# Kernel optimization log

Measured on AMD Instinct MI355X. Metric: run time of the kernel, lower is better.

## Reference

```python
import jax, jax.numpy as jnp
import numpy as np

N = 100000   # nodes
E = 1600000  # edges
R = 500      # relation types
D = 128      # in_ent_feats == out_ent_feats
H = 8        # heads
Dh = 16      # head dim
DFF = 4 * D  # feed-forward hidden
HOPS = 5
ALPHA = 0.15
SLOPE = 0.2
EPS = 1e-5


def setup_inputs() -> dict:
    key = jax.random.key(0)
    ks = jax.random.split(key, 12)
    s = 0.05  # small-init scale
    return {
        "ent_feat": jax.random.normal(ks[0], (N, D), jnp.float32),
        "rel_feat": jax.random.normal(ks[1], (R, D), jnp.float32),
        "src": jax.random.randint(ks[2], (E,), 0, N),
        "dst": jax.random.randint(ks[3], (E,), 0, N),
        "e_type": jax.random.randint(ks[4], (E,), 0, R),
        "ln1_g": jnp.ones((D,), jnp.float32),
        "ln1_b": jnp.zeros((D,), jnp.float32),
        "W_ent": jax.random.normal(ks[5], (D, H * Dh), jnp.float32) * s,
        "W_rel": jax.random.normal(ks[6], (D, H * Dh), jnp.float32) * s,
        "attn_h": jax.random.normal(ks[7], (1, H, Dh), jnp.float32) * s,
        "attn_t": jax.random.normal(ks[8], (1, H, Dh), jnp.float32) * s,
        "attn_r": jax.random.normal(ks[9], (1, H, Dh), jnp.float32) * s,
        "ln2_g": jnp.ones((H * Dh,), jnp.float32),
        "ln2_b": jnp.zeros((H * Dh,), jnp.float32),
        "W1": jax.random.normal(ks[10], (H * Dh, DFF), jnp.float32) * s,
        "b1": jnp.zeros((DFF,), jnp.float32),
        "W2": jax.random.normal(ks[11], (DFF, H * Dh), jnp.float32) * s,
        "b2": jnp.zeros((H * Dh,), jnp.float32),
    }


def _ln(x, g, b):
    mu = x.mean(-1, keepdims=True)
    var = x.var(-1, keepdims=True)
    return (x - mu) * jax.lax.rsqrt(var + EPS) * g + b


def reference(ent_feat, rel_feat, src, dst, e_type,
              ln1_g, ln1_b, W_ent, W_rel, attn_h, attn_t, attn_r,
              ln2_g, ln2_b, W1, b1, W2, b2):
    # graph layer norm (dropout is identity at eval)
    h = _ln(ent_feat, ln1_g, ln1_b)                       # [N, D]
    feat = (h @ W_ent).reshape(N, H, Dh)                  # [N, H, Dh]
    frel = (rel_feat @ W_rel).reshape(R, H, Dh)           # [R, H, Dh]
    eh = (feat * attn_h).sum(-1)                          # [N, H]
    et = (feat * attn_t).sum(-1)                          # [N, H]
    er = (frel * attn_r).sum(-1)[e_type]                  # [E, H]
    # edge scores: u_add_v + relation term, leaky relu
    e = eh[src] + et[dst] + er                            # [E, H]
    e = jnp.where(e > 0, e, SLOPE * e)
    # edge softmax over incoming edges of each dst node
    m = jax.ops.segment_max(e, dst, num_segments=N)       # [N, H]
    ex = jnp.exp(e - m[dst])
    ssum = jax.ops.segment_sum(ex, dst, num_segments=N)
    a = ex / ssum[dst]                                    # [E, H]
    # PPR diffusion
    feat0 = feat
    f = feat0
    for _ in range(HOPS):
        msg = f[src] * a[:, :, None]                      # [E, H, Dh]
        agg = jax.ops.segment_sum(msg, dst, num_segments=N)
        f = (1.0 - ALPHA) * agg + ALPHA * feat0
    # residual (Identity since in == out)
    rst = f + h.reshape(N, H, Dh)
    rst = rst.reshape(N, H * Dh)
    # feed-forward sublayer with residual
    y = _ln(rst, ln2_g, ln2_b)
    ff = jax.nn.relu(y @ W1 + b1) @ W2 + b2
    return ff + rst
```

## Files before the change

### kernel.cpp

```cpp
#include <hip/hip_runtime.h>
#include <hip/hip_bf16.h>
#include <math.h>

#define N_NODES 100000
#define N_EDGES 1600000
#define N_REL   500
#define DIM     128
#define NHEAD   8
#define DFF     512
#define ALPHA   0.15f
#define SLOPE   0.2f
#define LN_EPS  1e-5f

#define SCHUNK   1024
#define NSCANBLK ((N_NODES + SCHUNK - 1) / SCHUNK)

#define NWIN    8
#define WNODES  12500
#define NECHUNK 256
#define ECHUNK  (N_EDGES / NECHUNK)

#define FNODES  16

typedef unsigned short u16;
typedef unsigned int   u32;

typedef __attribute__((ext_vector_type(8))) short  bf16x8;
typedef __attribute__((ext_vector_type(4))) float  f32x4;

__device__ __forceinline__ float bf2f(u16 u) {
    return __uint_as_float(((u32)u) << 16);
}
__device__ __forceinline__ u16 f2bf(float f) {
    __hip_bfloat16 b = __float2bfloat16(f);
    return *reinterpret_cast<u16*>(&b);
}

__global__ void zero_k(int* __restrict__ p, int n) {
    int i = blockIdx.x * blockDim.x + threadIdx.x;
    if (i < n) p[i] = 0;
}

__global__ void swz1_k(const float* __restrict__ W1, u16* __restrict__ W1s) {
    const int i = blockIdx.x * 256 + threadIdx.x;
    const int k = i >> 9, n = i & 511;
    W1s[n * DIM + k] = f2bf(W1[i]);
}
__global__ void swz2_k(const float* __restrict__ W2, u16* __restrict__ W2s) {
    const int i = blockIdx.x * 256 + threadIdx.x;
    const int k = i >> 7, n = i & 127;
    W2s[n * DFF + k] = f2bf(W2[i]);
}
__global__ void swze_k(const float* __restrict__ W, u16* __restrict__ Ws) {
    const int i = blockIdx.x * 256 + threadIdx.x;
    const int k = i >> 7, n = i & 127;
    Ws[n * DIM + k] = f2bf(W[i]);
}

__global__ __launch_bounds__(128) void ln1_k(const float* __restrict__ x,
        const float* __restrict__ g, const float* __restrict__ b,
        float* __restrict__ h) {
    const int n = blockIdx.x, t = threadIdx.x;
    const float v = x[n * DIM + t];
    float s = v, q = v * v;
#pragma unroll
    for (int off = 32; off > 0; off >>= 1) {
        s += __shfl_xor(s, off, 64);
        q += __shfl_xor(q, off, 64);
    }
    __shared__ float ss[2], qq[2];
    if ((t & 63) == 0) { ss[t >> 6] = s; qq[t >> 6] = q; }
    __syncthreads();
    s = ss[0] + ss[1]; q = qq[0] + qq[1];
    const float mu  = s * (1.0f / 128.0f);
    const float var = q * (1.0f / 128.0f) - mu * mu;
    const float rs  = rsqrtf(fmaxf(var, 0.f) + LN_EPS);
    h[n * DIM + t] = (v - mu) * rs * g[t] + b[t];
}

#define HP 136
__global__ __launch_bounds__(256) void proj_k(const float* __restrict__ h,
        const u16* __restrict__ Wes,
        u16* __restrict__ feat0) {
    __shared__ u16 hsb[32 * HP];
    const int t   = threadIdx.x;
    const int n0b = blockIdx.x * 32;

    {
        const int sr = t >> 3;
        const int sc = (t & 7) * 16;
        const float* hrow = &h[(size_t)(n0b + sr) * DIM + sc];
        u16* drow = &hsb[sr * HP + sc];
#pragma unroll
        for (int i = 0; i < 4; ++i) {
            const float4 hv = ((const float4*)hrow)[i];
            ushort4 o;
            o.x = f2bf(hv.x); o.y = f2bf(hv.y); o.z = f2bf(hv.z); o.w = f2bf(hv.w);
            ((ushort4*)drow)[i] = o;
        }
    }
    __syncthreads();

    const int wv   = t >> 6;
    const int lane = t & 63;
    const int lm   = lane & 15;
    const int q4   = lane >> 4;
    const int mrow = (wv & 1) * 16;
    const int chalf = (wv >> 1) * 64;

    bf16x8 afr[4];
#pragma unroll
    for (int kt = 0; kt < 4; ++kt)
        afr[kt] = *(const bf16x8*)&hsb[(mrow + lm) * HP + kt * 32 + q4 * 8];

#pragma unroll
    for (int nt = 0; nt < 4; ++nt) {
        const int c0 = chalf + nt * 16;
        f32x4 acc = {0.f, 0.f, 0.f, 0.f};
#pragma unroll
        for (int kt = 0; kt < 4; ++kt) {
            const bf16x8 bfr = *(const bf16x8*)&Wes[(c0 + lm) * DIM + kt * 32 + q4 * 8];
            acc = __builtin_amdgcn_mfma_f32_16x16x32_bf16(afr[kt], bfr, acc, 0, 0, 0);
        }
#pragma unroll
        for (int r = 0; r < 4; ++r)
            feat0[(size_t)(n0b + mrow + q4 * 4 + r) * DIM + c0 + lm] = f2bf(acc[r]);
    }
}

__global__ __launch_bounds__(256) void eh_k(const u16* __restrict__ feat0,
        const float* __restrict__ attn_h, const float* __restrict__ attn_t,
        float* __restrict__ eh, float* __restrict__ et) {
    __shared__ float ahs[DIM], ats[DIM];
    const int t = threadIdx.x;
    if (t < DIM) { ahs[t] = attn_h[t]; ats[t] = attn_t[t]; }
    __syncthreads();
    const int idx  = blockIdx.x * 256 + t;
    const int n    = idx >> 3;
    const int head = idx & 7;
    const u16* fp = &feat0[(size_t)n * DIM + head * 16];
    float sh = 0.f, st = 0.f;
#pragma unroll
    for (int i = 0; i < 4; ++i) {
        const ushort4 f4 = ((const ushort4*)fp)[i];
        const int c = head * 16 + i * 4;
        sh += bf2f(f4.x) * ahs[c+0] + bf2f(f4.y) * ahs[c+1]
            + bf2f(f4.z) * ahs[c+2] + bf2f(f4.w) * ahs[c+3];
        st += bf2f(f4.x) * ats[c+0] + bf2f(f4.y) * ats[c+1]
            + bf2f(f4.z) * ats[c+2] + bf2f(f4.w) * ats[c+3];
    }
    eh[idx] = sh;
    et[idx] = st;
}

__global__ __launch_bounds__(128) void rel_k(const float* __restrict__ rel_feat,
        const float* __restrict__ W,
        const float* __restrict__ attn_r, float* __restrict__ er) {
    __shared__ float rf[DIM];
    __shared__ float pr[DIM];
    const int r = blockIdx.x, t = threadIdx.x;
    rf[t] = rel_feat[r * DIM + t];
    __syncthreads();
    float acc = 0.f;
    for (int d = 0; d < DIM; ++d) acc += rf[d] * W[d * DIM + t];
    pr[t] = acc * attn_r[t];
    __syncthreads();
    if (t < NHEAD) {
        float s = 0.f;
        for (int i = 0; i < 16; ++i) s += pr[t * 16 + i];
        er[r * NHEAD + t] = s;
    }
}

__global__ void count_k(const int* __restrict__ dst, int* __restrict__ counts) {
    int e = blockIdx.x * blockDim.x + threadIdx.x;
    if (e < N_EDGES) atomicAdd(&counts[dst[e]], 1);
}

__global__ __launch_bounds__(256) void scan1_k(const int* __restrict__ counts,
        int* __restrict__ offsets, int* __restrict__ blk_sums, int n) {
    __shared__ int wsum[4];
    const int t = threadIdx.x, lane = t & 63, wid = t >> 6;
    const int base = blockIdx.x * SCHUNK + t * 4;
    int v0 = 0, v1 = 0, v2 = 0, v3 = 0;
    if (base + 3 < n) {
        const int4 c4 = *(const int4*)&counts[base];
        v0 = c4.x; v1 = c4.y; v2 = c4.z; v3 = c4.w;
    } else {
        if (base + 0 < n) v0 = counts[base + 0];
        if (base + 1 < n) v1 = counts[base + 1];
        if (base + 2 < n) v2 = counts[base + 2];
        if (base + 3 < n) v3 = counts[base + 3];
    }
    const int s4 = v0 + v1 + v2 + v3;
    int incl = s4;
#pragma unroll
    for (int off = 1; off < 64; off <<= 1) {
        const int tt = __shfl_up(incl, off, 64);
        if (lane >= off) incl += tt;
    }
    if (lane == 63) wsum[wid] = incl;
    __syncthreads();
    int wbase = 0;
#pragma unroll
    for (int w = 0; w < 4; ++w) if (w < wid) wbase += wsum[w];
    const int excl = wbase + incl - s4;
    if (base + 0 < n) offsets[base + 0] = excl;
    if (base + 1 < n) offsets[base + 1] = excl + v0;
    if (base + 2 < n) offsets[base + 2] = excl + v0 + v1;
    if (base + 3 < n) offsets[base + 3] = excl + v0 + v1 + v2;
    if (t == 255) blk_sums[blockIdx.x] = wbase + incl;
}

__global__ __launch_bounds__(128) void scan2_k(const int* __restrict__ blk_sums,
        int* __restrict__ blk_off, int* __restrict__ offsets, int nblk, int n) {
    const int t = threadIdx.x;
    const int v = (t < nblk) ? blk_sums[t] : 0;
    int incl = v;
#pragma unroll
    for (int off = 1; off < 64; off <<= 1) {
        const int tt = __shfl_up(incl, off, 64);
        if ((t & 63) >= off) incl += tt;
    }
    __shared__ int w0sum;
    if (t == 63) w0sum = incl;
    __syncthreads();
    int x = incl - v;
    if (t >= 64) x += w0sum;
    if (t < nblk) blk_off[t] = x;
    if (t == nblk - 1) offsets[n] = x + v;
}

__global__ __launch_bounds__(256) void scan3_k(int* __restrict__ offsets,
        int* __restrict__ cursor, const int* __restrict__ blk_off, int n) {
    const int add  = blk_off[blockIdx.x];
    const int base = blockIdx.x * SCHUNK + threadIdx.x * 4;
#pragma unroll
    for (int j = 0; j < 4; ++j) {
        const int i = base + j;
        if (i < n) {
            const int o = offsets[i] + add;
            offsets[i] = o;
            cursor[i]  = o;
        }
    }
}

__global__ __launch_bounds__(256) void scatter_k(const int* __restrict__ src,
        const int* __restrict__ dst, const int* __restrict__ etype,
        int* __restrict__ cursor, u32* __restrict__ csr_se) {
    const int b  = blockIdx.x;
    const int w  = b & (NWIN - 1);
    const int r  = b >> 3;
    const int lo = w * WNODES, hi = lo + WNODES;
    const int base = r * ECHUNK;
    for (int i = threadIdx.x; i < ECHUNK; i += 256) {
        const int e = base + i;
        const int d = dst[e];
        if (d >= lo && d < hi) {
            const int s   = src[e];
            const int rel = etype[e];
            const int pos = atomicAdd(&cursor[d], 1);
            if (pos >= 0 && pos < N_EDGES)
                csr_se[pos] = (u32)s | ((u32)rel << 17);
        }
    }
}

__global__ __launch_bounds__(256) void softmax_k(const int* __restrict__ offsets,
        const u32* __restrict__ csr_se,
        const float* __restrict__ eh, const float* __restrict__ et,
        const float* __restrict__ er,
        u16* __restrict__ csr_ab, float* __restrict__ inv_buf) {
    const int n = blockIdx.x * 4 + (threadIdx.x >> 6);
    const int beg = offsets[n], end = offsets[n + 1];
    const int lane = threadIdx.x & 63;
    const int k  = lane & 7;
    const int eo = lane >> 3;
    const float etk = et[n * NHEAD + k];
    float m = -1e30f;
    for (int e = beg + eo; e < end; e += 8) {
        const u32 se = csr_se[e];
        const int s = se & 0x1FFFF;
        const int r = se >> 17;
        float sc = eh[s * NHEAD + k] + etk + er[r * NHEAD + k];
        sc = sc > 0.f ? sc : SLOPE * sc;
        m = fmaxf(m, sc);
    }
    m = fmaxf(m, __shfl_xor(m, 8, 64));
    m = fmaxf(m, __shfl_xor(m, 16, 64));
    m = fmaxf(m, __shfl_xor(m, 32, 64));
    float ssum = 0.f;
    for (int e = beg + eo; e < end; e += 8) {
        const u32 se = csr_se[e];
        const int s = se & 0x1FFFF;
        const int r = se >> 17;
        float sc = eh[s * NHEAD + k] + etk + er[r * NHEAD + k];
        sc = sc > 0.f ? sc : SLOPE * sc;
        const float ex = expf(sc - m);
        csr_ab[(size_t)e * NHEAD + k] = f2bf(ex);
        ssum += ex;
    }
    ssum += __shfl_xor(ssum, 8, 64);
    ssum += __shfl_xor(ssum, 16, 64);
    ssum += __shfl_xor(ssum, 32, 64);
    const float inv = 1.f / fmaxf(ssum, 1e-20f);
    if (lane < 8) inv_buf[n * NHEAD + lane] = inv;
}

__global__ __launch_bounds__(256) void hop_k(const u16* __restrict__ f_in,
        u16* __restrict__ f_out, const u16* __restrict__ feat0,
        const int* __restrict__ offsets, const u32* __restrict__ csr_se,
        const u16* __restrict__ csr_ab, const float* __restrict__ inv_buf) {
    const int n    = blockIdx.x * 4 + (threadIdx.x >> 6);
    const int lane = threadIdx.x & 63;
    const int li   = lane & 15;
    const int grp  = lane >> 4;
    const int hsel = li >> 1;
    const int beg = offsets[n], end = offsets[n + 1];
    const int deg = end - beg;

    float acc[8];
#pragma unroll
    for (int j = 0; j < 8; ++j) acc[j] = 0.f;

    const int nfull = deg >> 4;
    int e0 = beg;
    for (int i = 0; i < nfull; ++i, e0 += 16) {
        const u32 se16 = csr_se[e0 + li];
#pragma unroll
        for (int u = 0; u < 4; ++u) {
            const int eu = e0 + u * 4 + grp;
            const u32 se = __shfl(se16, u * 4 + grp, 16);
            const int s  = (int)(se & 0x1FFFF);
            const float a = bf2f(csr_ab[(size_t)eu * NHEAD + hsel]);
            const bf16x8 row = *(const bf16x8*)&f_in[(size_t)s * DIM + li * 8];
#pragma unroll
            for (int j = 0; j < 8; ++j)
                acc[j] += a * bf2f((u16)row[j]);
        }
    }
    for (int e = e0 + grp; e < end; e += 4) {
        const u32 se = csr_se[e];
        const int s  = (int)(se & 0x1FFFF);
        const float a = bf2f(csr_ab[(size_t)e * NHEAD + hsel]);
        const bf16x8 row = *(const bf16x8*)&f_in[(size_t)s * DIM + li * 8];
#pragma unroll
        for (int j = 0; j < 8; ++j)
            acc[j] += a * bf2f((u16)row[j]);
    }
#pragma unroll
    for (int j = 0; j < 8; ++j) {
        acc[j] += __shfl_xor(acc[j], 16, 64);
        acc[j] += __shfl_xor(acc[j], 32, 64);
    }
    if (lane < 16) {
        const float iv = inv_buf[n * NHEAD + hsel];
        const bf16x8 p = *(const bf16x8*)&feat0[(size_t)n * DIM + li * 8];
        bf16x8 o;
#pragma unroll
        for (int j = 0; j < 8; ++j)
            o[j] = (short)f2bf((1.f - ALPHA) * acc[j] * iv + ALPHA * bf2f((u16)p[j]));
        *(bf16x8*)&f_out[(size_t)n * DIM + li * 8] = o;
    }
}

#define YP 136
#define ZP 520
__global__ __launch_bounds__(256) void ffn_k(const u16* __restrict__ f,
        const float* __restrict__ h,
        const float* __restrict__ g2, const float* __restrict__ b2ln,
        const u16* __restrict__ W1s,
        const float* __restrict__ b1,
        const u16* __restrict__ W2s,
        const float* __restrict__ b2,
        float* __restrict__ out) {
    __shared__ u16 ysb[FNODES * YP];
    __shared__ u16 zsb[FNODES * ZP];

    const int t    = threadIdx.x;
    const int n0b  = blockIdx.x * FNODES;
    const int wv   = t >> 6;
    const int lane = t & 63;

    {
        const int node = t >> 4;
        const int cp   = (t & 15) * 8;
        const int gbase = (n0b + node) * DIM + cp;
        const ushort4 fu0 = *(const ushort4*)&f[gbase];
        const ushort4 fu1 = *(const ushort4*)&f[gbase + 4];
        const float4  hv0 = *(const float4*)&h[gbase];
        const float4  hv1 = *(const float4*)&h[gbase + 4];
        float rv[8];
        rv[0] = bf2f(fu0.x) + hv0.x; rv[1] = bf2f(fu0.y) + hv0.y;
        rv[2] = bf2f(fu0.z) + hv0.z; rv[3] = bf2f(fu0.w) + hv0.w;
        rv[4] = bf2f(fu1.x) + hv1.x; rv[5] = bf2f(fu1.y) + hv1.y;
        rv[6] = bf2f(fu1.z) + hv1.z; rv[7] = bf2f(fu1.w) + hv1.w;
        float s = 0.f, q = 0.f;
#pragma unroll
        for (int i = 0; i < 8; ++i) { s += rv[i]; q += rv[i] * rv[i]; }
        s += __shfl_xor(s, 1, 64); q += __shfl_xor(q, 1, 64);
        s += __shfl_xor(s, 2, 64); q += __shfl_xor(q, 2, 64);
        s += __shfl_xor(s, 4, 64); q += __shfl_xor(q, 4, 64);
        s += __shfl_xor(s, 8, 64); q += __shfl_xor(q, 8, 64);
        const float mu  = s * (1.0f / 128.0f);
        const float var = q * (1.0f / 128.0f) - mu * mu;
        const float rs  = rsqrtf(fmaxf(var, 0.f) + LN_EPS);
        ushort4 yo0, yo1;
        yo0.x = f2bf((rv[0] - mu) * rs * g2[cp+0] + b2ln[cp+0]);
        yo0.y = f2bf((rv[1] - mu) * rs * g2[cp+1] + b2ln[cp+1]);
        yo0.z = f2bf((rv[2] - mu) * rs * g2[cp+2] + b2ln[cp+2]);
        yo0.w = f2bf((rv[3] - mu) * rs * g2[cp+3] + b2ln[cp+3]);
        yo1.x = f2bf((rv[4] - mu) * rs * g2[cp+4] + b2ln[cp+4]);
        yo1.y = f2bf((rv[5] - mu) * rs * g2[cp+5] + b2ln[cp+5]);
        yo1.z = f2bf((rv[6] - mu) * rs * g2[cp+6] + b2ln[cp+6]);
        yo1.w = f2bf((rv[7] - mu) * rs * g2[cp+7] + b2ln[cp+7]);
        *(ushort4*)&ysb[node * YP + cp]     = yo0;
        *(ushort4*)&ysb[node * YP + cp + 4] = yo1;
    }
    __syncthreads();

    const int lm = lane & 15;
    const int q4 = lane >> 4;

    {
        bf16x8 afr[4];
#pragma unroll
        for (int kt = 0; kt < 4; ++kt)
            afr[kt] = *(const bf16x8*)&ysb[lm * YP + kt * 32 + q4 * 8];

        const int cw = wv * 128;
#pragma unroll
        for (int nt = 0; nt < 8; ++nt) {
            const int n0 = cw + nt * 16;
            f32x4 acc0 = {0.f, 0.f, 0.f, 0.f};
#pragma unroll
            for (int kt = 0; kt < 4; ++kt) {
                const bf16x8 bfr = *(const bf16x8*)&W1s[(n0 + lm) * DIM + kt * 32 + q4 * 8];
                acc0 = __builtin_amdgcn_mfma_f32_16x16x32_bf16(afr[kt], bfr, acc0, 0, 0, 0);
            }
            const float bias = b1[n0 + lm];
#pragma unroll
            for (int r = 0; r < 4; ++r)
                zsb[(q4 * 4 + r) * ZP + n0 + lm] = f2bf(fmaxf(acc0[r] + bias, 0.f));
        }
    }
    __syncthreads();

    f32x4 acc[2];
    acc[0] = (f32x4){0.f, 0.f, 0.f, 0.f};
    acc[1] = (f32x4){0.f, 0.f, 0.f, 0.f};
    const int c0 = wv * 32;
#pragma unroll
    for (int kt = 0; kt < 16; ++kt) {
        const bf16x8 a0  = *(const bf16x8*)&zsb[lm * ZP + kt * 32 + q4 * 8];
        const bf16x8 b0  = *(const bf16x8*)&W2s[(c0 + lm) * DFF + kt * 32 + q4 * 8];
        const bf16x8 b1f = *(const bf16x8*)&W2s[(c0 + 16 + lm) * DFF + kt * 32 + q4 * 8];
        acc[0] = __builtin_amdgcn_mfma_f32_16x16x32_bf16(a0, b0,  acc[0], 0, 0, 0);
        acc[1] = __builtin_amdgcn_mfma_f32_16x16x32_bf16(a0, b1f, acc[1], 0, 0, 0);
    }

#pragma unroll
    for (int ntile = 0; ntile < 2; ++ntile) {
        const int col = c0 + ntile * 16 + lm;
        const float bias = b2[col];
#pragma unroll
        for (int r = 0; r < 4; ++r) {
            const int row  = q4 * 4 + r;
            const int gidx = (n0b + row) * DIM + col;
            out[gidx] = acc[ntile][r] + bias + bf2f(f[gidx]) + h[gidx];
        }
    }
}

extern "C" void kernel_launch(void* const* d_in, const int* in_sizes, int n_in,
                              void* d_out, int out_size, void* d_ws, size_t ws_size,
                              hipStream_t stream) {
    const float* ent_feat = (const float*)d_in[0];
    const float* rel_feat = (const float*)d_in[1];
    const int*   src      = (const int*)d_in[2];
    const int*   dst      = (const int*)d_in[3];
    const int*   e_type   = (const int*)d_in[4];
    const float* ln1_g    = (const float*)d_in[5];
    const float* ln1_b    = (const float*)d_in[6];
    const float* W_ent    = (const float*)d_in[7];
    const float* W_rel    = (const float*)d_in[8];
    const float* attn_h   = (const float*)d_in[9];
    const float* attn_t   = (const float*)d_in[10];
    const float* attn_r   = (const float*)d_in[11];
    const float* ln2_g    = (const float*)d_in[12];
    const float* ln2_b    = (const float*)d_in[13];
    const float* W1       = (const float*)d_in[14];
    const float* b1       = (const float*)d_in[15];
    const float* W2       = (const float*)d_in[16];
    const float* b2       = (const float*)d_in[17];
    float* out = (float*)d_out;

    char* ws = (char*)d_ws;
    size_t used = 0;
    auto alloc = [&](size_t bytes) -> char* {
        char* p = ws + used;
        used += (bytes + 255) & ~(size_t)255;
        return p;
    };
    float* h       = (float*)alloc((size_t)N_NODES * DIM * 4);
    u16*   feat0   = (u16*)  alloc((size_t)N_NODES * DIM * 2);
    u16*   fA      = (u16*)  alloc((size_t)N_NODES * DIM * 2);
    u16*   fB      = (u16*)  alloc((size_t)N_NODES * DIM * 2);
    u16*   csr_ab  = (u16*)  alloc((size_t)N_EDGES * NHEAD * 2);
    float* eh      = (float*)alloc((size_t)N_NODES * NHEAD * 4);
    float* et      = (float*)alloc((size_t)N_NODES * NHEAD * 4);
    float* inv_buf = (float*)alloc((size_t)N_NODES * NHEAD * 4);
    u32*   csr_se  = (u32*)  alloc((size_t)N_EDGES * 4);
    int*   counts  = (int*)  alloc((size_t)N_NODES * 4);
    int*   offsets = (int*)  alloc((size_t)(N_NODES + 1) * 4);
    int*   cursor  = (int*)  alloc((size_t)N_NODES * 4);
    float* er      = (float*)alloc((size_t)N_REL * NHEAD * 4);
    u16*   W1s     = (u16*)  alloc((size_t)DIM * DFF * 2);
    u16*   W2s     = (u16*)  alloc((size_t)DFF * DIM * 2);
    u16*   Wes     = (u16*)  alloc((size_t)DIM * DIM * 2);
    int*   blk_sums= (int*)  alloc((size_t)NSCANBLK * 4);
    int*   blk_off = (int*)  alloc((size_t)NSCANBLK * 4);

    if (used > ws_size) return;

    swz1_k<<<DIM * DFF / 256, 256, 0, stream>>>(W1, W1s);
    swz2_k<<<DFF * DIM / 256, 256, 0, stream>>>(W2, W2s);
    swze_k<<<DIM * DIM / 256, 256, 0, stream>>>(W_ent, Wes);

    ln1_k<<<N_NODES, 128, 0, stream>>>(ent_feat, ln1_g, ln1_b, h);
    proj_k<<<N_NODES / 32, 256, 0, stream>>>(h, Wes, feat0);
    eh_k<<<N_NODES * NHEAD / 256, 256, 0, stream>>>(feat0, attn_h, attn_t, eh, et);
    rel_k<<<N_REL, 128, 0, stream>>>(rel_feat, W_rel, attn_r, er);

    zero_k<<<(N_NODES + 255) / 256, 256, 0, stream>>>(counts, N_NODES);
    count_k<<<(N_EDGES + 255) / 256, 256, 0, stream>>>(dst, counts);
    scan1_k<<<NSCANBLK, 256, 0, stream>>>(counts, offsets, blk_sums, N_NODES);
    scan2_k<<<1, 128, 0, stream>>>(blk_sums, blk_off, offsets, NSCANBLK, N_NODES);
    scan3_k<<<NSCANBLK, 256, 0, stream>>>(offsets, cursor, blk_off, N_NODES);
    scatter_k<<<NECHUNK * NWIN, 256, 0, stream>>>(src, dst, e_type,
                                                  cursor, csr_se);
    softmax_k<<<N_NODES / 4, 256, 0, stream>>>(offsets, csr_se, eh, et, er,
                                               csr_ab, inv_buf);

    hop_k<<<N_NODES / 4, 256, 0, stream>>>(feat0, fA, feat0, offsets, csr_se, csr_ab, inv_buf);
    hop_k<<<N_NODES / 4, 256, 0, stream>>>(fA, fB, feat0, offsets, csr_se, csr_ab, inv_buf);
    hop_k<<<N_NODES / 4, 256, 0, stream>>>(fB, fA, feat0, offsets, csr_se, csr_ab, inv_buf);
    hop_k<<<N_NODES / 4, 256, 0, stream>>>(fA, fB, feat0, offsets, csr_se, csr_ab, inv_buf);
    hop_k<<<N_NODES / 4, 256, 0, stream>>>(fB, fA, feat0, offsets, csr_se, csr_ab, inv_buf);

    ffn_k<<<N_NODES / FNODES, 256, 0, stream>>>(fA, h, ln2_g, ln2_b, W1s, b1, W2s, b2,
                                                out);
}
```

Before: 969.8 us.

## Process 32 nodes per FFN block with 8 waves to reuse weight fragments

The FFN kernel now handles 32 nodes per block with 512 threads (8 waves) instead of 16 nodes with 256 threads. Each W1 and W2 fragment loaded from global memory feeds two MFMA row tiles, which halves weight traffic per node. The prologue now covers 32 nodes with 512 threads. LDS use per block doubles, and the launch bounds hint may limit registers. Risk: N_NODES/32 = 3125 exactly, so there is no tail.

```diff
diff --git a/kernel.cpp b/kernel.cpp
--- a/kernel.cpp
+++ b/kernel.cpp
@@ -19,8 +19,6 @@
 #define WNODES  12500
 #define NECHUNK 256
 #define ECHUNK  (N_EDGES / NECHUNK)
-
-#define FNODES  16
 
 typedef unsigned short u16;
 typedef unsigned int   u32;
@@ -367,7 +365,7 @@
 
 #define YP 136
 #define ZP 520
-__global__ __launch_bounds__(256) void ffn_k(const u16* __restrict__ f,
+__global__ __launch_bounds__(512, 6) void ffn_k(const u16* __restrict__ f,
         const float* __restrict__ h,
         const float* __restrict__ g2, const float* __restrict__ b2ln,
         const u16* __restrict__ W1s,
@@ -375,11 +373,11 @@
         const u16* __restrict__ W2s,
         const float* __restrict__ b2,
         float* __restrict__ out) {
-    __shared__ u16 ysb[FNODES * YP];
-    __shared__ u16 zsb[FNODES * ZP];
+    __shared__ u16 ysb[32 * YP];
+    __shared__ u16 zsb[32 * ZP];
 
     const int t    = threadIdx.x;
-    const int n0b  = blockIdx.x * FNODES;
+    const int n0b  = blockIdx.x * 32;
     const int wv   = t >> 6;
     const int lane = t & 63;
 
@@ -424,25 +422,31 @@
     const int q4 = lane >> 4;
 
     {
-        bf16x8 afr[4];
-#pragma unroll
-        for (int kt = 0; kt < 4; ++kt)
-            afr[kt] = *(const bf16x8*)&ysb[lm * YP + kt * 32 + q4 * 8];
-
-        const int cw = wv * 128;
-#pragma unroll
-        for (int nt = 0; nt < 8; ++nt) {
+        bf16x8 afr[2][4];
+#pragma unroll
+        for (int mt = 0; mt < 2; ++mt)
+#pragma unroll
+            for (int kt = 0; kt < 4; ++kt)
+                afr[mt][kt] = *(const bf16x8*)&ysb[(mt * 16 + lm) * YP + kt * 32 + q4 * 8];
+
+        const int cw = wv * 64;
+#pragma unroll
+        for (int nt = 0; nt < 4; ++nt) {
             const int n0 = cw + nt * 16;
             f32x4 acc0 = {0.f, 0.f, 0.f, 0.f};
+            f32x4 acc1 = {0.f, 0.f, 0.f, 0.f};
 #pragma unroll
             for (int kt = 0; kt < 4; ++kt) {
                 const bf16x8 bfr = *(const bf16x8*)&W1s[(n0 + lm) * DIM + kt * 32 + q4 * 8];
-                acc0 = __builtin_amdgcn_mfma_f32_16x16x32_bf16(afr[kt], bfr, acc0, 0, 0, 0);
+                acc0 = __builtin_amdgcn_mfma_f32_16x16x32_bf16(afr[0][kt], bfr, acc0, 0, 0, 0);
+                acc1 = __builtin_amdgcn_mfma_f32_16x16x32_bf16(afr[1][kt], bfr, acc1, 0, 0, 0);
             }
             const float bias = b1[n0 + lm];
 #pragma unroll
-            for (int r = 0; r < 4; ++r)
-                zsb[(q4 * 4 + r) * ZP + n0 + lm] = f2bf(fmaxf(acc0[r] + bias, 0.f));
+            for (int r = 0; r < 4; ++r) {
+                zsb[(q4 * 4 + r) * ZP + n0 + lm]      = f2bf(fmaxf(acc0[r] + bias, 0.f));
+                zsb[(16 + q4 * 4 + r) * ZP + n0 + lm] = f2bf(fmaxf(acc1[r] + bias, 0.f));
+            }
         }
     }
     __syncthreads();
@@ -450,25 +454,27 @@
     f32x4 acc[2];
     acc[0] = (f32x4){0.f, 0.f, 0.f, 0.f};
     acc[1] = (f32x4){0.f, 0.f, 0.f, 0.f};
-    const int c0 = wv * 32;
+    const int c0 = wv * 16;
 #pragma unroll
     for (int kt = 0; kt < 16; ++kt) {
-        const bf16x8 a0  = *(const bf16x8*)&zsb[lm * ZP + kt * 32 + q4 * 8];
-        const bf16x8 b0  = *(const bf16x8*)&W2s[(c0 + lm) * DFF + kt * 32 + q4 * 8];
-        const bf16x8 b1f = *(const bf16x8*)&W2s[(c0 + 16 + lm) * DFF + kt * 32 + q4 * 8];
-        acc[0] = __builtin_amdgcn_mfma_f32_16x16x32_bf16(a0, b0,  acc[0], 0, 0, 0);
-        acc[1] = __builtin_amdgcn_mfma_f32_16x16x32_bf16(a0, b1f, acc[1], 0, 0, 0);
-    }
-
-#pragma unroll
-    for (int ntile = 0; ntile < 2; ++ntile) {
-        const int col = c0 + ntile * 16 + lm;
+        const bf16x8 a0 = *(const bf16x8*)&zsb[lm * ZP + kt * 32 + q4 * 8];
+        const bf16x8 a1 = *(const bf16x8*)&zsb[(16 + lm) * ZP + kt * 32 + q4 * 8];
+        const bf16x8 b0 = *(const bf16x8*)&W2s[(c0 + lm) * DFF + kt * 32 + q4 * 8];
+        acc[0] = __builtin_amdgcn_mfma_f32_16x16x32_bf16(a0, b0, acc[0], 0, 0, 0);
+        acc[1] = __builtin_amdgcn_mfma_f32_16x16x32_bf16(a1, b0, acc[1], 0, 0, 0);
+    }
+
+    {
+        const int col = c0 + lm;
         const float bias = b2[col];
 #pragma unroll
-        for (int r = 0; r < 4; ++r) {
-            const int row  = q4 * 4 + r;
-            const int gidx = (n0b + row) * DIM + col;
-            out[gidx] = acc[ntile][r] + bias + bf2f(f[gidx]) + h[gidx];
+        for (int mt = 0; mt < 2; ++mt) {
+#pragma unroll
+            for (int r = 0; r < 4; ++r) {
+                const int row  = mt * 16 + q4 * 4 + r;
+                const int gidx = (n0b + row) * DIM + col;
+                out[gidx] = acc[mt][r] + bias + bf2f(f[gidx]) + h[gidx];
+            }
         }
     }
 }
@@ -549,6 +555,6 @@
     hop_k<<<N_NODES / 4, 256, 0, stream>>>(fA, fB, feat0, offsets, csr_se, csr_ab, inv_buf);
     hop_k<<<N_NODES / 4, 256, 0, stream>>>(fB, fA, feat0, offsets, csr_se, csr_ab, inv_buf);
 
-    ffn_k<<<N_NODES / FNODES, 256, 0, stream>>>(fA, h, ln2_g, ln2_b, W1s, b1, W2s, b2,
-                                                out);
-}
+    ffn_k<<<N_NODES / 32, 512, 0, stream>>>(fA, h, ln2_g, ln2_b, W1s, b1, W2s, b2,
+                                            out);
+}
```

Result: faster. 905.3 us (-6.6%).
